# Performance work log

Hardware: AMD Instinct MI355X
Metric: run time of the kernel (lower is better)

## Reference

```python
import jax, jax.numpy as jnp
import numpy as np

B, CIN, COUT, N, T, K = 16, 32, 64, 1024, 64, 3


def setup_inputs() -> dict:
    key = jax.random.key(0)
    k1, k2, k3 = jax.random.split(key, 3)
    x = jax.random.normal(k1, (B, CIN, N, T), dtype=jnp.float32)
    # scaled laplacian-like support (keep spectral radius ~1 so Chebyshev terms stay bounded)
    adj = jax.random.normal(k2, (N, N), dtype=jnp.float32) / np.sqrt(N).astype(np.float32)
    W = jax.random.normal(k3, (4 * COUT, (CIN + COUT) * K), dtype=jnp.float32) * 0.02
    b = jnp.zeros((4 * COUT,), dtype=jnp.float32)
    return {"x": x, "adj": adj, "W": W, "b": b}


def reference(x, adj, W, b):
    Bn, cin, Nn, Tn = x.shape
    c_out = W.shape[0] // 4
    feat_in = W.shape[1] // K  # = cin + c_out

    # Chebyshev polynomial basis of adj (loop-invariant across time; compute once)
    Ls = [jnp.eye(Nn, dtype=x.dtype), adj]
    for _ in range(2, K):
        Ls.append(2.0 * (adj @ Ls[-1]) - Ls[-2])
    Lap = jnp.stack(Ls, 0)  # [K, N, N]; Ls[k][q, n]

    # Conv1d(kernel=1) weight reshaped to match channel flatten order (c major, k minor)
    Wr = W.reshape(4 * c_out, feat_in, K)  # [4*c_out, F, K]
    bb = b[None, :, None]

    def step(carry, xt):
        h, c = carry
        tem = jnp.concatenate([xt, h], axis=1)  # [B, F, N]
        # einsum('bcn,knq->bckq', x, Lap.T) == einsum('bfn,kqn->bfkq', x, Lap)
        g = jnp.einsum('bfn,kqn->bfkq', tem, Lap)  # [B, F, K, N]
        fea = jnp.einsum('bfkq,ofk->boq', g, Wr) + bb  # [B, 4*c_out, N]
        i, j, f, o = jnp.split(fea, 4, axis=1)
        new_c = c * jax.nn.sigmoid(f) + jax.nn.sigmoid(i) * jnp.tanh(j)
        new_h = jnp.tanh(new_c) * jax.nn.sigmoid(o)
        return (new_h, new_c), new_h

    h0 = jnp.zeros((Bn, c_out, Nn), dtype=x.dtype)
    c0 = jnp.zeros((Bn, c_out, Nn), dtype=x.dtype)
    x_t = jnp.moveaxis(x, -1, 0)  # [T, B, cin, N]
    _, outs = jax.lax.scan(step, (h0, c0), x_t)  # [T, B, c_out, N]
    return jnp.moveaxis(outs, 0, -1)  # [B, c_out, N, T]
```

## Files before the change

### kernel.cpp

```cpp
#include <hip/hip_runtime.h>
#include <stdint.h>


#define Bb   16
#define CIN  32
#define COUT 64
#define Nn   1024
#define Tt   64
#define Ff   96
#define G4   256
#define KJ   288

#define BUFSZ 65536
#define AOLO  12288
#define BOHI  24576
#define BOLO  40960
#define GQPB  624
#define GQLO  39936

typedef unsigned short u16;
typedef short short8 __attribute__((ext_vector_type(8)));
typedef short short4v __attribute__((ext_vector_type(4)));
typedef float f32x4 __attribute__((ext_vector_type(4)));

static __device__ __forceinline__ u16 f2bf(float f) {
    union { float f; uint32_t u; } v; v.f = f;
    uint32_t r = v.u + 0x7FFFu + ((v.u >> 16) & 1u);
    return (u16)(r >> 16);
}
static __device__ __forceinline__ float bf2f(u16 h) {
    union { uint32_t u; float f; } v; v.u = ((uint32_t)h) << 16;
    return v.f;
}
static __device__ __forceinline__ float sigm(float x) { return 1.0f / (1.0f + expf(-x)); }

static __device__ __forceinline__ void gload16(const void* g, void* l) {
    __builtin_amdgcn_global_load_lds(
        (const __attribute__((address_space(1))) void*)g,
        (__attribute__((address_space(3))) void*)l, 16, 0, 0);
}

__global__ void k_fill(float* out, int n, float v) {
    int i = blockIdx.x * 256 + threadIdx.x;
    if (i < n) out[i] = v;
}

__global__ __launch_bounds__(256) void k_adj_split(const float* __restrict__ adj,
                                                   u16* __restrict__ hi, u16* __restrict__ lo) {
    int i = blockIdx.x * 256 + threadIdx.x;
    float v = adj[i];
    u16 h = f2bf(v);
    hi[i] = h; lo[i] = f2bf(v - bf2f(h));
}

__global__ __launch_bounds__(256) void k_adj_t(const float* __restrict__ adj,
                                               u16* __restrict__ th, u16* __restrict__ tl_) {
    __shared__ float tile[64][65];
    int m0 = blockIdx.x * 64, n0 = blockIdx.y * 64;
    int tid = threadIdx.x;
    #pragma unroll
    for (int i = 0; i < 16; i++) {
        int lin = i * 256 + tid;
        int ml = lin >> 6, nl = lin & 63;
        tile[ml][nl] = adj[(size_t)(m0 + ml) * Nn + n0 + nl];
    }
    __syncthreads();
    #pragma unroll
    for (int i = 0; i < 16; i++) {
        int lin = i * 256 + tid;
        int nl = lin >> 6, ml = lin & 63;
        float v = tile[ml][nl];
        u16 h = f2bf(v);
        size_t off = (size_t)(n0 + nl) * Nn + m0 + ml;
        th[off] = h; tl_[off] = f2bf(v - bf2f(h));
    }
}

__global__ __launch_bounds__(256) void k_l2(
    const u16* __restrict__ a_hi, const u16* __restrict__ a_lo,
    const u16* __restrict__ bt_hi, const u16* __restrict__ bt_lo,
    u16* __restrict__ o_hi, u16* __restrict__ o_lo)
{
    __shared__ u16 Ah[64][40], Al[64][40], Bh[64][40], Bl[64][40];
    const int tid = threadIdx.x, lane = tid & 63, w = tid >> 6;
    const int wm = (w >> 1) * 32, wn = (w & 1) * 32;
    const int r0 = blockIdx.x * 64, q0 = blockIdx.y * 64;
    const int srow = tid >> 2, scol = (tid & 3) * 8;
    const u16* arh = a_hi + (size_t)(r0 + srow) * Nn;
    const u16* arl = a_lo + (size_t)(r0 + srow) * Nn;
    const u16* brh = bt_hi + (size_t)(q0 + srow) * Nn;
    const u16* brl = bt_lo + (size_t)(q0 + srow) * Nn;

    f32x4 acc[2][2];
    #pragma unroll
    for (int i = 0; i < 2; i++)
        #pragma unroll
        for (int j = 0; j < 2; j++) acc[i][j] = (f32x4){0.f, 0.f, 0.f, 0.f};

    for (int k0 = 0; k0 < Nn; k0 += 32) {
        __syncthreads();
        *(short8*)&Ah[srow][scol] = *(const short8*)&arh[k0 + scol];
        *(short8*)&Al[srow][scol] = *(const short8*)&arl[k0 + scol];
        *(short8*)&Bh[srow][scol] = *(const short8*)&brh[k0 + scol];
        *(short8*)&Bl[srow][scol] = *(const short8*)&brl[k0 + scol];
        __syncthreads();
        const int kb = (lane >> 4) * 8;
        short8 ah[2], al[2], bh[2], bl[2];
        #pragma unroll
        for (int mi = 0; mi < 2; mi++) {
            int row = wm + mi * 16 + (lane & 15);
            ah[mi] = *(const short8*)&Ah[row][kb];
            al[mi] = *(const short8*)&Al[row][kb];
        }
        #pragma unroll
        for (int ni = 0; ni < 2; ni++) {
            int col = wn + ni * 16 + (lane & 15);
            bh[ni] = *(const short8*)&Bh[col][kb];
            bl[ni] = *(const short8*)&Bl[col][kb];
        }
        #pragma unroll
        for (int mi = 0; mi < 2; mi++)
            #pragma unroll
            for (int ni = 0; ni < 2; ni++) {
                acc[mi][ni] = __builtin_amdgcn_mfma_f32_16x16x32_bf16(ah[mi], bh[ni], acc[mi][ni], 0, 0, 0);
                acc[mi][ni] = __builtin_amdgcn_mfma_f32_16x16x32_bf16(al[mi], bh[ni], acc[mi][ni], 0, 0, 0);
                acc[mi][ni] = __builtin_amdgcn_mfma_f32_16x16x32_bf16(ah[mi], bl[ni], acc[mi][ni], 0, 0, 0);
            }
    }
    #pragma unroll
    for (int mi = 0; mi < 2; mi++)
        #pragma unroll
        for (int ni = 0; ni < 2; ni++)
            #pragma unroll
            for (int j = 0; j < 4; j++) {
                int rr = r0 + wm + mi * 16 + (lane >> 4) * 4 + j;
                int qq = q0 + wn + ni * 16 + (lane & 15);
                float v = 2.f * acc[mi][ni][j] - ((rr == qq) ? 1.f : 0.f);
                size_t off = (size_t)rr * Nn + qq;
                u16 hh = f2bf(v);
                o_hi[off] = hh; o_lo[off] = f2bf(v - bf2f(hh));
            }
}

__global__ __launch_bounds__(256) void k_w_split(const float* __restrict__ W,
                                                 u16* __restrict__ hi, u16* __restrict__ lo) {
    int idx = blockIdx.x * 256 + threadIdx.x;
    int o = idx / KJ, j = idx - o * KJ;
    int k = j / Ff, f = j - k * Ff;
    float v = W[(size_t)o * KJ + f * 3 + k];
    u16 h = f2bf(v);
    hi[idx] = h; lo[idx] = f2bf(v - bf2f(h));
}

__global__ __launch_bounds__(256) void k_x_split(const float* __restrict__ x,
        u16* __restrict__ xf_hi, u16* __restrict__ xf_lo) {
    __shared__ float tile[64][65];
    int n0 = blockIdx.x * 64;
    int bc = blockIdx.y;
    const float* src = x + (size_t)bc * Nn * Tt;
    int tid = threadIdx.x;
    #pragma unroll
    for (int i = 0; i < 16; i++) {
        int lin = i * 256 + tid;
        int nl = lin >> 6, tl = lin & 63;
        tile[nl][tl] = src[(size_t)(n0 + nl) * Tt + tl];
    }
    __syncthreads();
    int b = bc >> 5, ch = bc & 31;
    #pragma unroll
    for (int i = 0; i < 2; i++) {
        int item = i * 256 + tid;
        int tl = item >> 3, oct = item & 7;
        short8 vh, vl;
        #pragma unroll
        for (int m = 0; m < 8; m++) {
            float v = tile[oct * 8 + m][tl];
            u16 h = f2bf(v);
            vh[m] = (short)h;
            vl[m] = (short)f2bf(v - bf2f(h));
        }
        size_t off = (((size_t)tl * Bb + b) * CIN + ch) * Nn + n0 + oct * 8;
        *(short8*)&xf_hi[off] = vh;
        *(short8*)&xf_lo[off] = vl;
    }
}

__global__ __launch_bounds__(1024, 4) void k_step(
    int t,
    const u16* __restrict__ xsf_hi, const u16* __restrict__ xsf_lo,
    u16* __restrict__ hf_hi, u16* __restrict__ hf_lo,
    const u16* __restrict__ bcat_hi, const u16* __restrict__ bcat_lo,
    const u16* __restrict__ Wh, const u16* __restrict__ Wl,
    const float* __restrict__ bias, float* __restrict__ cbuf,
    float* __restrict__ outbuf)
{
    __shared__ __attribute__((aligned(16))) char lds[131072];
    const int tid = threadIdx.x, lane = tid & 63, w = tid >> 6;
    const int bid = blockIdx.x;
    const int swz = (bid & 7) * 32 + (bid >> 3);
    const int qt = swz >> 4;
    const int bb = swz & 15;
    const int q0g = qt * 64;

    const u16* srcb[4];
    #pragma unroll
    for (int i = 0; i < 4; i++) {
        int u = i * 1024 + tid;
        if (u < 1536) {
            int hl = (u >= 768) ? 1 : 0;
            int r = (u - hl * 768) >> 3, c8 = u & 7;
            const u16* p;
            if (r < CIN) p = (hl ? xsf_lo : xsf_hi) + (size_t)((t * Bb + bb) * CIN + r) * Nn;
            else         p = (hl ? hf_lo  : hf_hi ) + (size_t)(bb * COUT + r - CIN) * Nn;
            srcb[i] = p + (c8 ^ (r & 7)) * 8;
        } else if (u < 3584) {
            int v = u - 1536;
            int hl = v >> 10;
            int r = (v & 1023) >> 3, c8 = v & 7;
            int grow = q0g + (r & 63) + ((r >= 64) ? Nn : 0);
            srcb[i] = (hl ? bcat_lo : bcat_hi) + (size_t)grow * Nn + (c8 ^ (r & 7)) * 8;
        } else {
            srcb[i] = bcat_hi + (u & 1023) * 8;
        }
    }

    const int wr = w >> 3, wc = w & 7;
    f32x4 acc[3];
    #pragma unroll
    for (int i = 0; i < 3; i++) acc[i] = (f32x4){0.f, 0.f, 0.f, 0.f};

    u16 cxh[6], cxl[6];
    #pragma unroll
    for (int i = 0; i < 6; i++) { cxh[i] = 0; cxl[i] = 0; }

    #pragma unroll
    for (int i = 0; i < 4; i++)
        gload16(srcb[i], lds + (i * 1024 + tid) * 16);

    for (int kc = 0; kc < 16; kc++) {
        if (kc < 15) {
            char* nb = lds + ((kc + 1) & 1) * BUFSZ;
            const int k0 = (kc + 1) * 64;
            #pragma unroll
            for (int i = 0; i < 4; i++)
                gload16(srcb[i] + k0, nb + (i * 1024 + tid) * 16);
            asm volatile("s_waitcnt vmcnt(4)" ::: "memory");
        } else {
            asm volatile("s_waitcnt vmcnt(0)" ::: "memory");
        }
        __builtin_amdgcn_s_barrier();
        const char* bo = lds + (kc & 1) * BUFSZ;
        #pragma unroll
        for (int kk = 0; kk < 2; kk++) {
            const int ksw = kk * 4 + (lane >> 4);
            short8 ah[3], al[3], bh, bl;
            #pragma unroll
            for (int mi = 0; mi < 3; mi++) {
                int r = wr * 48 + mi * 16 + (lane & 15);
                int off = r * 128 + ((ksw ^ (r & 7)) << 4);
                ah[mi] = *(const short8*)(bo + off);
                al[mi] = *(const short8*)(bo + AOLO + off);
            }
            {
                int rb = wc * 16 + (lane & 15);
                int off = rb * 128 + ((ksw ^ (rb & 7)) << 4);
                bh = *(const short8*)(bo + BOHI + off);
                bl = *(const short8*)(bo + BOLO + off);
            }
            #pragma unroll
            for (int mi = 0; mi < 3; mi++) {
                acc[mi] = __builtin_amdgcn_mfma_f32_16x16x32_bf16(ah[mi], bh, acc[mi], 0, 0, 0);
                acc[mi] = __builtin_amdgcn_mfma_f32_16x16x32_bf16(al[mi], bh, acc[mi], 0, 0, 0);
                acc[mi] = __builtin_amdgcn_mfma_f32_16x16x32_bf16(ah[mi], bl, acc[mi], 0, 0, 0);
            }
        }
        if (kc == qt) {
            #pragma unroll
            for (int jj = 0; jj < 6; jj++) {
                int j = w * 6 + jj;
                int off = j * 128 + ((((lane >> 3)) ^ (j & 7)) << 4) + (lane & 7) * 2;
                cxh[jj] = *(const u16*)(bo + off);
                cxl[jj] = *(const u16*)(bo + AOLO + off);
            }
            asm volatile("s_waitcnt lgkmcnt(0)" ::: "memory");
            __builtin_amdgcn_sched_barrier(0);
        }
        __builtin_amdgcn_s_barrier();
    }

    {
        #pragma unroll
        for (int jj = 0; jj < 6; jj++) {
            int j = w * 6 + jj;
            *(u16*)(lds + lane * GQPB + j * 2) = cxh[jj];
            *(u16*)(lds + GQLO + lane * GQPB + j * 2) = cxl[jj];
        }
    }
    #pragma unroll
    for (int mi = 0; mi < 3; mi++) {
        int c = wc * 16 + (lane & 15);
        int g = c >> 6, ql = c & 63;
        int f0 = wr * 48 + mi * 16 + (lane >> 4) * 4;
        int jd = 96 + g * 96 + f0;
        short4v vh, vl;
        #pragma unroll
        for (int j = 0; j < 4; j++) {
            float v = acc[mi][j];
            u16 hh = f2bf(v);
            vh[j] = (short)hh;
            vl[j] = (short)f2bf(v - bf2f(hh));
        }
        *(short4v*)(lds + ql * GQPB + jd * 2) = vh;
        *(short4v*)(lds + GQLO + ql * GQPB + jd * 2) = vl;
    }
    __syncthreads();

    f32x4 a2[2][2];
    #pragma unroll
    for (int i = 0; i < 2; i++)
        #pragma unroll
        for (int j = 0; j < 2; j++) a2[i][j] = (f32x4){0.f, 0.f, 0.f, 0.f};

    const int wo = w >> 1, wq = w & 1;
    const int kb8 = (lane >> 4) * 8;
    #pragma unroll
    for (int c = 0; c < 9; c++) {
        int j0 = c * 32;
        short8 wh[2], wl2[2], gh[2], gl[2];
        #pragma unroll
        for (int mi = 0; mi < 2; mi++) {
            int o = wo * 32 + mi * 16 + (lane & 15);
            size_t so = (size_t)o * KJ + j0 + kb8;
            wh[mi]  = *(const short8*)&Wh[so];
            wl2[mi] = *(const short8*)&Wl[so];
        }
        #pragma unroll
        for (int ni = 0; ni < 2; ni++) {
            int q = wq * 32 + ni * 16 + (lane & 15);
            int off = q * GQPB + (j0 + kb8) * 2;
            gh[ni] = *(const short8*)(lds + off);
            gl[ni] = *(const short8*)(lds + GQLO + off);
        }
        #pragma unroll
        for (int mi = 0; mi < 2; mi++)
            #pragma unroll
            for (int ni = 0; ni < 2; ni++) {
                a2[mi][ni] = __builtin_amdgcn_mfma_f32_16x16x32_bf16(wh[mi],  gh[ni], a2[mi][ni], 0, 0, 0);
                a2[mi][ni] = __builtin_amdgcn_mfma_f32_16x16x32_bf16(wl2[mi], gh[ni], a2[mi][ni], 0, 0, 0);
                a2[mi][ni] = __builtin_amdgcn_mfma_f32_16x16x32_bf16(wh[mi],  gl[ni], a2[mi][ni], 0, 0, 0);
            }
    }
    __syncthreads();

    {
        float* FEAf = (float*)lds;
        #pragma unroll
        for (int mi = 0; mi < 2; mi++) {
            int o0 = wo * 32 + mi * 16 + (lane >> 4) * 4;
            f32x4 bv = *(const f32x4*)&bias[o0];
            #pragma unroll
            for (int ni = 0; ni < 2; ni++) {
                int q = wq * 32 + ni * 16 + (lane & 15);
                #pragma unroll
                for (int j = 0; j < 4; j++)
                    FEAf[(o0 + j) * 65 + q] = a2[mi][ni][j] + bv[j];
            }
        }
    }
    __syncthreads();

    {
        const float* FEAf = (const float*)lds;
        int q = tid & 63, qg = q0g + q;
        int co0 = (tid >> 6) * 4;
        #pragma unroll
        for (int ii = 0; ii < 4; ii++) {
            int co = co0 + ii;
            float iv = FEAf[co * 65 + q];
            float jv = FEAf[(co + 64) * 65 + q];
            float fv = FEAf[(co + 128) * 65 + q];
            float ov = FEAf[(co + 192) * 65 + q];
            size_t cof = ((size_t)(bb * COUT + co)) * Nn + qg;
            float cc = cbuf[cof];
            float nc = cc * sigm(fv) + sigm(iv) * tanhf(jv);
            float nh = tanhf(nc) * sigm(ov);
            cbuf[cof] = nc;
            u16 hh = f2bf(nh);
            hf_hi[cof] = hh; hf_lo[cof] = f2bf(nh - bf2f(hh));
            outbuf[((size_t)(t * Bb + bb) * COUT + co) * Nn + qg] = nh;
        }
    }
}

__global__ __launch_bounds__(256) void k_out_t(const float* __restrict__ outbuf,
                                               float* __restrict__ out) {
    __shared__ float tile[64][65];
    int q0 = blockIdx.x * 64;
    int bo = blockIdx.y;
    int b = bo >> 6, o = bo & 63;
    int tid = threadIdx.x;
    #pragma unroll
    for (int i = 0; i < 16; i++) {
        int lin = i * 256 + tid;
        int tl = lin >> 6, ql = lin & 63;
        tile[tl][ql] = outbuf[(((size_t)tl * Bb + b) * COUT + o) * Nn + q0 + ql];
    }
    __syncthreads();
    #pragma unroll
    for (int i = 0; i < 16; i++) {
        int lin = i * 256 + tid;
        int ql = lin >> 6, tl = lin & 63;
        out[((size_t)bo * Nn + q0 + ql) * Tt + tl] = tile[tl][ql];
    }
}

extern "C" void kernel_launch(void* const* d_in, const int* in_sizes, int n_in,
                              void* d_out, int out_size, void* d_ws, size_t ws_size,
                              hipStream_t stream)
{
    const float* x    = (const float*)d_in[0];
    const float* adj  = (const float*)d_in[1];
    const float* W    = (const float*)d_in[2];
    const float* bias = (const float*)d_in[3];
    float* out = (float*)d_out;

    size_t off = 0;
    char* base = (char*)d_ws;
    auto take = [&](size_t bytes) -> void* {
        void* r = base + off;
        off += (bytes + 255) & ~(size_t)255;
        return r;
    };
    u16* bcat_hi = (u16*)take(2ull * 2 * Nn * Nn);
    u16* bcat_lo = (u16*)take(2ull * 2 * Nn * Nn);
    u16* adjT_hi = (u16*)take(2ull * Nn * Nn);
    u16* adjT_lo = (u16*)take(2ull * Nn * Nn);
    u16* xsf_hi  = (u16*)take(2ull * Tt * Bb * CIN * Nn);
    u16* xsf_lo  = (u16*)take(2ull * Tt * Bb * CIN * Nn);
    u16* hf_hi   = (u16*)take(2ull * Bb * COUT * Nn);
    u16* hf_lo   = (u16*)take(2ull * Bb * COUT * Nn);
    float* cbuf  = (float*)take(4ull * Bb * COUT * Nn);
    u16* Wc_hi   = (u16*)take(2ull * G4 * KJ);
    u16* Wc_lo   = (u16*)take(2ull * G4 * KJ);
    float* outbuf = (float*)take(4ull * (size_t)Tt * Bb * COUT * Nn);

    if (off > ws_size) {
        float v = (float)(ws_size >> 20);
        k_fill<<<dim3((out_size + 255) / 256), 256, 0, stream>>>(out, out_size, v);
        return;
    }

    hipMemsetAsync(hf_hi, 0, 2ull * Bb * COUT * Nn, stream);
    hipMemsetAsync(hf_lo, 0, 2ull * Bb * COUT * Nn, stream);
    hipMemsetAsync(cbuf, 0, 4ull * Bb * COUT * Nn, stream);

    k_adj_split<<<dim3((Nn * Nn) / 256), 256, 0, stream>>>(adj, bcat_hi, bcat_lo);
    k_adj_t<<<dim3(16, 16), 256, 0, stream>>>(adj, adjT_hi, adjT_lo);
    k_l2<<<dim3(16, 16), 256, 0, stream>>>(bcat_hi, bcat_lo, adjT_hi, adjT_lo,
                                           bcat_hi + (size_t)Nn * Nn, bcat_lo + (size_t)Nn * Nn);
    k_w_split<<<dim3((G4 * KJ) / 256), 256, 0, stream>>>(W, Wc_hi, Wc_lo);
    k_x_split<<<dim3(Nn / 64, Bb * CIN), 256, 0, stream>>>(x, xsf_hi, xsf_lo);

    for (int t = 0; t < Tt; t++) {
        k_step<<<dim3(256), 1024, 0, stream>>>(t,
            xsf_hi, xsf_lo, hf_hi, hf_lo,
            bcat_hi, bcat_lo, Wc_hi, Wc_lo,
            bias, cbuf, outbuf);
    }
    k_out_t<<<dim3(Nn / 64, Bb * COUT), 256, 0, stream>>>(outbuf, out);
}
```

Measured before the change: 2.783 ms.

## Split K across wave groups in graph GEMM with LDS reduction

Re-partitions the 16 waves of the graph-propagation GEMM. Each wave now computes a larger 48x32 output tile over half of every 64-wide K chunk, instead of a 48x16 tile over the full chunk. This improves register reuse of the A and B fragments and reduces LDS fragment loads per MFMA. The cost is an extra LDS scratch round-trip with two barriers to sum the two K halves, and more accumulator registers per wave, which may hurt occupancy.

```diff
diff --git a/kernel.cpp b/kernel.cpp
--- a/kernel.cpp
+++ b/kernel.cpp
@@ -17,6 +17,7 @@
 #define BOLO  40960
 #define GQPB  624
 #define GQLO  39936
+#define SCP   97
 
 typedef unsigned short u16;
 typedef short short8 __attribute__((ext_vector_type(8)));
@@ -224,10 +225,16 @@
         }
     }
 
-    const int wr = w >> 3, wc = w & 7;
-    f32x4 acc[3];
-    #pragma unroll
-    for (int i = 0; i < 3; i++) acc[i] = (f32x4){0.f, 0.f, 0.f, 0.f};
+    const int kg = w >> 3;
+    const int wsub = w & 7;
+    const int wr = wsub >> 2, wc = wsub & 3;
+    const int ksw = kg * 4 + (lane >> 4);
+
+    f32x4 acc[3][2];
+    #pragma unroll
+    for (int i = 0; i < 3; i++)
+        #pragma unroll
+        for (int j = 0; j < 2; j++) acc[i][j] = (f32x4){0.f, 0.f, 0.f, 0.f};
 
     u16 cxh[6], cxl[6];
     #pragma unroll
@@ -250,10 +257,8 @@
         }
         __builtin_amdgcn_s_barrier();
         const char* bo = lds + (kc & 1) * BUFSZ;
-        #pragma unroll
-        for (int kk = 0; kk < 2; kk++) {
-            const int ksw = kk * 4 + (lane >> 4);
-            short8 ah[3], al[3], bh, bl;
+        {
+            short8 ah[3], al[3], bh[2], bl[2];
             #pragma unroll
             for (int mi = 0; mi < 3; mi++) {
                 int r = wr * 48 + mi * 16 + (lane & 15);
@@ -261,18 +266,21 @@
                 ah[mi] = *(const short8*)(bo + off);
                 al[mi] = *(const short8*)(bo + AOLO + off);
             }
-            {
-                int rb = wc * 16 + (lane & 15);
+            #pragma unroll
+            for (int ni = 0; ni < 2; ni++) {
+                int rb = wc * 32 + ni * 16 + (lane & 15);
                 int off = rb * 128 + ((ksw ^ (rb & 7)) << 4);
-                bh = *(const short8*)(bo + BOHI + off);
-                bl = *(const short8*)(bo + BOLO + off);
-            }
-            #pragma unroll
-            for (int mi = 0; mi < 3; mi++) {
-                acc[mi] = __builtin_amdgcn_mfma_f32_16x16x32_bf16(ah[mi], bh, acc[mi], 0, 0, 0);
-                acc[mi] = __builtin_amdgcn_mfma_f32_16x16x32_bf16(al[mi], bh, acc[mi], 0, 0, 0);
-                acc[mi] = __builtin_amdgcn_mfma_f32_16x16x32_bf16(ah[mi], bl, acc[mi], 0, 0, 0);
-            }
+                bh[ni] = *(const short8*)(bo + BOHI + off);
+                bl[ni] = *(const short8*)(bo + BOLO + off);
+            }
+            #pragma unroll
+            for (int mi = 0; mi < 3; mi++)
+                #pragma unroll
+                for (int ni = 0; ni < 2; ni++) {
+                    acc[mi][ni] = __builtin_amdgcn_mfma_f32_16x16x32_bf16(ah[mi], bh[ni], acc[mi][ni], 0, 0, 0);
+                    acc[mi][ni] = __builtin_amdgcn_mfma_f32_16x16x32_bf16(al[mi], bh[ni], acc[mi][ni], 0, 0, 0);
+                    acc[mi][ni] = __builtin_amdgcn_mfma_f32_16x16x32_bf16(ah[mi], bl[ni], acc[mi][ni], 0, 0, 0);
+                }
         }
         if (kc == qt) {
             #pragma unroll
@@ -289,6 +297,32 @@
     }
 
     {
+        float* scratch = (float*)lds;
+        if (kg == 0) {
+            #pragma unroll
+            for (int mi = 0; mi < 3; mi++)
+                #pragma unroll
+                for (int ni = 0; ni < 2; ni++) {
+                    int c = wc * 32 + ni * 16 + (lane & 15);
+                    int r0 = wr * 48 + mi * 16 + (lane >> 4) * 4;
+                    *(f32x4*)&scratch[c * SCP + r0] = acc[mi][ni];
+                }
+        }
+        __syncthreads();
+        if (kg == 1) {
+            #pragma unroll
+            for (int mi = 0; mi < 3; mi++)
+                #pragma unroll
+                for (int ni = 0; ni < 2; ni++) {
+                    int c = wc * 32 + ni * 16 + (lane & 15);
+                    int r0 = wr * 48 + mi * 16 + (lane >> 4) * 4;
+                    acc[mi][ni] += *(const f32x4*)&scratch[c * SCP + r0];
+                }
+        }
+        __syncthreads();
+    }
+
+    {
         #pragma unroll
         for (int jj = 0; jj < 6; jj++) {
             int j = w * 6 + jj;
@@ -296,22 +330,26 @@
             *(u16*)(lds + GQLO + lane * GQPB + j * 2) = cxl[jj];
         }
     }
-    #pragma unroll
-    for (int mi = 0; mi < 3; mi++) {
-        int c = wc * 16 + (lane & 15);
-        int g = c >> 6, ql = c & 63;
-        int f0 = wr * 48 + mi * 16 + (lane >> 4) * 4;
-        int jd = 96 + g * 96 + f0;
-        short4v vh, vl;
-        #pragma unroll
-        for (int j = 0; j < 4; j++) {
-            float v = acc[mi][j];
-            u16 hh = f2bf(v);
-            vh[j] = (short)hh;
-            vl[j] = (short)f2bf(v - bf2f(hh));
-        }
-        *(short4v*)(lds + ql * GQPB + jd * 2) = vh;
-        *(short4v*)(lds + GQLO + ql * GQPB + jd * 2) = vl;
+    if (kg == 1) {
+        #pragma unroll
+        for (int mi = 0; mi < 3; mi++)
+            #pragma unroll
+            for (int ni = 0; ni < 2; ni++) {
+                int c = wc * 32 + ni * 16 + (lane & 15);
+                int g = c >> 6, ql = c & 63;
+                int f0 = wr * 48 + mi * 16 + (lane >> 4) * 4;
+                int jd = 96 + g * 96 + f0;
+                short4v vh, vl;
+                #pragma unroll
+                for (int j = 0; j < 4; j++) {
+                    float v = acc[mi][ni][j];
+                    u16 hh = f2bf(v);
+                    vh[j] = (short)hh;
+                    vl[j] = (short)f2bf(v - bf2f(hh));
+                }
+                *(short4v*)(lds + ql * GQPB + jd * 2) = vh;
+                *(short4v*)(lds + GQLO + ql * GQPB + jd * 2) = vl;
+            }
     }
     __syncthreads();
 
```

After: 2.866 ms. 1.03x slower.
